# Kernel optimization log

Measured on AMD Instinct MI355X. Metric: run time of the kernel, lower is better.

## Reference

```python
import jax, jax.numpy as jnp
import numpy as np

N_NODES = 50000


def gcn_conv(x, W, b, src, dst, n_nodes):
    """PyG GCNConv: add self-loops, symmetric deg normalization, x@W then aggregate."""
    h = x @ W  # [N, out]
    # add self loops
    loop = jnp.arange(n_nodes, dtype=src.dtype)
    s = jnp.concatenate([src, loop])
    d = jnp.concatenate([dst, loop])
    # degree at target nodes (includes self loop)
    deg = jax.ops.segment_sum(jnp.ones_like(d, dtype=h.dtype), d, num_segments=n_nodes)
    dinv = jnp.where(deg > 0, jax.lax.rsqrt(deg), 0.0)
    norm = dinv[s] * dinv[d]  # [E+N]
    msgs = h[s] * norm[:, None]  # [E+N, out]
    out = jax.ops.segment_sum(msgs, d, num_segments=n_nodes)
    return out + b


def setup_inputs() -> dict:
    key = jax.random.key(0)
    k = jax.random.split(key, 8)
    d_in, d_h, d_z = 128, 128, 32
    x = jax.random.normal(k[0], (N_NODES, d_in), dtype=jnp.float32)
    edge_index = jax.random.randint(k[1], (2, 600000), 0, N_NODES, dtype=jnp.int64)
    y_edge_index = jax.random.randint(k[2], (2, 200000), 0, N_NODES, dtype=jnp.int64)
    W1 = jax.random.normal(k[3], (d_in, d_h), dtype=jnp.float32) / np.sqrt(d_in)
    b1 = jnp.zeros((d_h,), dtype=jnp.float32)
    W_mu = jax.random.normal(k[4], (d_h, d_z), dtype=jnp.float32) / np.sqrt(d_h)
    b_mu = jnp.zeros((d_z,), dtype=jnp.float32)
    W_ls = jax.random.normal(k[5], (d_h, d_z), dtype=jnp.float32) / np.sqrt(d_h)
    b_ls = jnp.zeros((d_z,), dtype=jnp.float32)
    return {"x": x, "edge_index": edge_index, "y_edge_index": y_edge_index,
            "W1": W1, "b1": b1, "W_mu": W_mu, "b_mu": b_mu, "W_ls": W_ls, "b_ls": b_ls}


def reference(x, edge_index, y_edge_index, W1, b1, W_mu, b_mu, W_ls, b_ls):
    ei = jnp.concatenate([edge_index, y_edge_index], axis=1)
    src, dst = ei[0], ei[1]
    n = x.shape[0]
    h = jax.nn.relu(gcn_conv(x, W1, b1, src, dst, n))
    z_mu = gcn_conv(h, W_mu, b_mu, src, dst, n)
    z_logstd = gcn_conv(h, W_ls, b_ls, src, dst, n)
    return (z_mu, z_logstd)
```

## Files before the change

### kernel.cpp

```cpp
#include <hip/hip_runtime.h>
#include <hip/hip_bf16.h>

#define CAP 64
#define NODES_PER_BLOCK 4

typedef __attribute__((ext_vector_type(8))) short short8;
typedef __attribute__((ext_vector_type(4))) float f32x4;

__device__ __forceinline__ unsigned short f2bf(float f) {
    unsigned int u = __float_as_uint(f);
    unsigned int r = (u + 0x7fffu + ((u >> 16) & 1u)) >> 16;
    return (unsigned short)r;
}
__device__ __forceinline__ float bf_lo(unsigned int u) { return __uint_as_float(u << 16); }
__device__ __forceinline__ float bf_hi(unsigned int u) { return __uint_as_float(u & 0xffff0000u); }

__global__ void fill_edges_kernel(const int* __restrict__ e1,
                                  const int* __restrict__ e2,
                                  int* __restrict__ counts, int* __restrict__ edges,
                                  int E1, int E2) {
    int e = blockIdx.x * blockDim.x + threadIdx.x;
    int s, d;
    if (e < E1) {
        s = e1[e]; d = e1[E1 + e];
    } else if (e < E1 + E2) {
        int t = e - E1;
        s = e2[t]; d = e2[E2 + t];
    } else return;
    int pos = atomicAdd(&counts[d], 1);
    if (pos < CAP) edges[d * CAP + pos] = s;
}

__global__ void dinv_kernel(const int* __restrict__ counts, float* __restrict__ dinv, int n) {
    int i = blockIdx.x * blockDim.x + threadIdx.x;
    if (i < n) dinv[i] = rsqrtf((float)(counts[i] + 1));
}

template <typename AT, int NT>
__global__ __launch_bounds__(256) void gemm_mfma_kernel(
    const AT* __restrict__ A, const float* __restrict__ Wa, const float* __restrict__ Wb,
    const float* __restrict__ dinv, unsigned short* __restrict__ C, int M) {
    constexpr int N   = NT * 16;
    constexpr int LDT = 136;
    __shared__ unsigned short As[64 * LDT];
    __shared__ unsigned short Ws[N * LDT];
    int tid  = threadIdx.x;
    int lane = tid & 63, w = tid >> 6;
    int brow = blockIdx.x * 64;

    if constexpr (sizeof(AT) == 4) {
        for (int it = 0; it < 8; ++it) {
            int idx = it * 256 + tid;
            int row = idx >> 5, c4 = idx & 31;
            int gr = brow + row;
            float4 v = make_float4(0.f, 0.f, 0.f, 0.f);
            if (gr < M) v = ((const float4*)(A + (size_t)gr * 128))[c4];
            ushort4 o; o.x = f2bf(v.x); o.y = f2bf(v.y); o.z = f2bf(v.z); o.w = f2bf(v.w);
            *(ushort4*)(As + row * LDT + c4 * 4) = o;
        }
    } else {
        for (int it = 0; it < 4; ++it) {
            int idx = it * 256 + tid;
            int row = idx >> 4, c8 = idx & 15;
            int gr = brow + row;
            short8 v = {};
            if (gr < M) v = ((const short8*)(A + (size_t)gr * 128))[c8];
            *(short8*)(As + row * LDT + c8 * 8) = v;
        }
    }
    if constexpr (NT == 8) {
        for (int it = 0; it < 16; ++it) {
            int idx = it * 256 + tid;
            int k = idx >> 5, q = idx & 31;
            float4 v = ((const float4*)(Wa + (size_t)k * 128))[q];
            int c = q * 4;
            Ws[(c + 0) * LDT + k] = f2bf(v.x);
            Ws[(c + 1) * LDT + k] = f2bf(v.y);
            Ws[(c + 2) * LDT + k] = f2bf(v.z);
            Ws[(c + 3) * LDT + k] = f2bf(v.w);
        }
    } else {
        for (int it = 0; it < 8; ++it) {
            int idx = it * 256 + tid;
            int k = idx >> 4, q = idx & 15;
            float4 v = (q < 8) ? ((const float4*)(Wa + (size_t)k * 32))[q]
                               : ((const float4*)(Wb + (size_t)k * 32))[q - 8];
            int c = q * 4;
            Ws[(c + 0) * LDT + k] = f2bf(v.x);
            Ws[(c + 1) * LDT + k] = f2bf(v.y);
            Ws[(c + 2) * LDT + k] = f2bf(v.z);
            Ws[(c + 3) * LDT + k] = f2bf(v.w);
        }
    }
    __syncthreads();

    f32x4 acc[NT] = {};
    int r = lane & 15, g = lane >> 4;
    const unsigned short* arow = As + (16 * w + r) * LDT + 8 * g;
#pragma unroll
    for (int kk = 0; kk < 4; ++kk) {
        short8 a = *(const short8*)(arow + 32 * kk);
#pragma unroll
        for (int ct = 0; ct < NT; ++ct) {
            short8 b = *(const short8*)(Ws + (ct * 16 + r) * LDT + 32 * kk + 8 * g);
            acc[ct] = __builtin_amdgcn_mfma_f32_16x16x32_bf16(a, b, acc[ct], 0, 0, 0);
        }
    }

#pragma unroll
    for (int ct = 0; ct < NT; ++ct) {
#pragma unroll
        for (int rr = 0; rr < 4; ++rr) {
            int row = brow + 16 * w + 4 * g + rr;
            if (row < M) {
                float sc = dinv[row];
                C[(size_t)row * N + ct * 16 + r] = f2bf(sc * acc[ct][rr]);
            }
        }
    }
}

__global__ void agg_h_kernel(const unsigned short* __restrict__ h1, const int* __restrict__ edges,
                             const int* __restrict__ counts, const float* __restrict__ dinv,
                             const float* __restrict__ b1, unsigned short* __restrict__ h, int n) {
    int wave = threadIdx.x >> 6, lane = threadIdx.x & 63;
    int v = blockIdx.x * NODES_PER_BLOCK + wave;
    if (v >= n) return;
    int cnt = min(counts[v], CAP);
    const int* el = edges + (size_t)v * CAP;
    float ax = 0.f, ay = 0.f;
#pragma unroll 4
    for (int e = 0; e < cnt; ++e) {
        int s = el[e];
        unsigned int u = ((const unsigned int*)(h1 + (size_t)s * 128))[lane];
        ax += bf_lo(u);
        ay += bf_hi(u);
    }
    unsigned int su = ((const unsigned int*)(h1 + (size_t)v * 128))[lane];
    ax += bf_lo(su);
    ay += bf_hi(su);
    float di = dinv[v];
    float ox = di * ax + b1[2 * lane];
    float oy = di * ay + b1[2 * lane + 1];
    unsigned int pack = (unsigned int)f2bf(fmaxf(ox, 0.f)) |
                        ((unsigned int)f2bf(fmaxf(oy, 0.f)) << 16);
    ((unsigned int*)(h + (size_t)v * 128))[lane] = pack;
}

__global__ void agg_out_kernel(const unsigned short* __restrict__ g, const int* __restrict__ edges,
                               const int* __restrict__ counts, const float* __restrict__ dinv,
                               const float* __restrict__ bmu, const float* __restrict__ bls,
                               float* __restrict__ out, int n) {
    int wave = threadIdx.x >> 6, lane = threadIdx.x & 63;
    int v = blockIdx.x * NODES_PER_BLOCK + wave;
    if (v >= n) return;
    int cnt = min(counts[v], CAP);
    const int* el = edges + (size_t)v * CAP;
    float acc = 0.f;
#pragma unroll 4
    for (int e = 0; e < cnt; ++e) {
        int s = el[e];
        acc += __uint_as_float((unsigned int)g[(size_t)s * 64 + lane] << 16);
    }
    acc += __uint_as_float((unsigned int)g[(size_t)v * 64 + lane] << 16);
    float res = dinv[v] * acc;
    if (lane < 32) {
        out[(size_t)v * 32 + lane] = res + bmu[lane];
    } else {
        out[(size_t)n * 32 + (size_t)v * 32 + (lane - 32)] = res + bls[lane - 32];
    }
}

extern "C" void kernel_launch(void* const* d_in, const int* in_sizes, int n_in,
                              void* d_out, int out_size, void* d_ws, size_t ws_size,
                              hipStream_t stream) {
    const float* x   = (const float*)d_in[0];
    const int*   ei  = (const int*)d_in[1];
    const int*   yei = (const int*)d_in[2];
    const float* W1  = (const float*)d_in[3];
    const float* b1  = (const float*)d_in[4];
    const float* Wmu = (const float*)d_in[5];
    const float* bmu = (const float*)d_in[6];
    const float* Wls = (const float*)d_in[7];
    const float* bls = (const float*)d_in[8];

    const int N  = in_sizes[0] / 128;
    const int E1 = in_sizes[1] / 2;
    const int E2 = in_sizes[2] / 2;
    const int E  = E1 + E2;

    size_t off = 0;
    auto alloc = [&](size_t bytes) {
        char* p = (char*)d_ws + off;
        off += (bytes + 255) & ~(size_t)255;
        return (void*)p;
    };
    int*            counts = (int*)alloc((size_t)N * 4);
    float*          dinv   = (float*)alloc((size_t)N * 4);
    int*            edges  = (int*)alloc((size_t)N * CAP * 4);
    unsigned short* h1     = (unsigned short*)alloc((size_t)N * 128 * 2);
    unsigned short* h      = (unsigned short*)alloc((size_t)N * 128 * 2);
    unsigned short* g      = h1;
    (void)ws_size; (void)n_in; (void)out_size;

    const int NB_N = (N + 255) / 256;
    const int NB_E = (E + 255) / 256;
    const int NB_G = (N + 63) / 64;

    hipMemsetAsync(counts, 0, (size_t)N * 4, stream);
    fill_edges_kernel<<<NB_E, 256, 0, stream>>>(ei, yei, counts, edges, E1, E2);
    dinv_kernel<<<NB_N, 256, 0, stream>>>(counts, dinv, N);

    gemm_mfma_kernel<float, 8><<<NB_G, 256, 0, stream>>>(x, W1, nullptr, dinv, h1, N);
    agg_h_kernel<<<(N + NODES_PER_BLOCK - 1) / NODES_PER_BLOCK, 64 * NODES_PER_BLOCK, 0, stream>>>(
        h1, edges, counts, dinv, b1, h, N);

    gemm_mfma_kernel<unsigned short, 4><<<NB_G, 256, 0, stream>>>(h, Wmu, Wls, dinv, g, N);
    agg_out_kernel<<<(N + NODES_PER_BLOCK - 1) / NODES_PER_BLOCK, 64 * NODES_PER_BLOCK, 0, stream>>>(
        g, edges, counts, dinv, bmu, bls, (float*)d_out, N);
}
```

Before: 251.3 us.

## Fuse edge fill with first GEMM, use 16-bit edge lists, inline degree norms

```diff
diff --git a/kernel.cpp b/kernel.cpp
--- a/kernel.cpp
+++ b/kernel.cpp
@@ -15,147 +15,144 @@
 __device__ __forceinline__ float bf_lo(unsigned int u) { return __uint_as_float(u << 16); }
 __device__ __forceinline__ float bf_hi(unsigned int u) { return __uint_as_float(u & 0xffff0000u); }
 
-__global__ void fill_edges_kernel(const int* __restrict__ e1,
-                                  const int* __restrict__ e2,
-                                  int* __restrict__ counts, int* __restrict__ edges,
-                                  int E1, int E2) {
-    int e = blockIdx.x * blockDim.x + threadIdx.x;
-    int s, d;
-    if (e < E1) {
-        s = e1[e]; d = e1[E1 + e];
-    } else if (e < E1 + E2) {
-        int t = e - E1;
-        s = e2[t]; d = e2[E2 + t];
-    } else return;
-    int pos = atomicAdd(&counts[d], 1);
-    if (pos < CAP) edges[d * CAP + pos] = s;
-}
-
-__global__ void dinv_kernel(const int* __restrict__ counts, float* __restrict__ dinv, int n) {
-    int i = blockIdx.x * blockDim.x + threadIdx.x;
-    if (i < n) dinv[i] = rsqrtf((float)(counts[i] + 1));
-}
-
-template <typename AT, int NT>
-__global__ __launch_bounds__(256) void gemm_mfma_kernel(
-    const AT* __restrict__ A, const float* __restrict__ Wa, const float* __restrict__ Wb,
-    const float* __restrict__ dinv, unsigned short* __restrict__ C, int M) {
-    constexpr int N   = NT * 16;
-    constexpr int LDT = 136;
-    __shared__ unsigned short As[64 * LDT];
-    __shared__ unsigned short Ws[N * LDT];
-    int tid  = threadIdx.x;
-    int lane = tid & 63, w = tid >> 6;
-    int brow = blockIdx.x * 64;
-
-    if constexpr (sizeof(AT) == 4) {
-        for (int it = 0; it < 8; ++it) {
-            int idx = it * 256 + tid;
-            int row = idx >> 5, c4 = idx & 31;
-            int gr = brow + row;
-            float4 v = make_float4(0.f, 0.f, 0.f, 0.f);
-            if (gr < M) v = ((const float4*)(A + (size_t)gr * 128))[c4];
-            ushort4 o; o.x = f2bf(v.x); o.y = f2bf(v.y); o.z = f2bf(v.z); o.w = f2bf(v.w);
-            *(ushort4*)(As + row * LDT + c4 * 4) = o;
-        }
+__global__ void prep_wt_kernel(const float* __restrict__ W1, const float* __restrict__ Wmu,
+                               const float* __restrict__ Wls,
+                               unsigned short* __restrict__ W1T, unsigned short* __restrict__ W2T) {
+    int idx = blockIdx.x * 256 + threadIdx.x;
+    if (idx < 128 * 128) {
+        int c = idx >> 7, k = idx & 127;
+        W1T[c * 128 + k] = f2bf(W1[k * 128 + c]);
     } else {
-        for (int it = 0; it < 4; ++it) {
-            int idx = it * 256 + tid;
-            int row = idx >> 4, c8 = idx & 15;
-            int gr = brow + row;
-            short8 v = {};
-            if (gr < M) v = ((const short8*)(A + (size_t)gr * 128))[c8];
-            *(short8*)(As + row * LDT + c8 * 8) = v;
-        }
-    }
-    if constexpr (NT == 8) {
-        for (int it = 0; it < 16; ++it) {
-            int idx = it * 256 + tid;
-            int k = idx >> 5, q = idx & 31;
-            float4 v = ((const float4*)(Wa + (size_t)k * 128))[q];
-            int c = q * 4;
-            Ws[(c + 0) * LDT + k] = f2bf(v.x);
-            Ws[(c + 1) * LDT + k] = f2bf(v.y);
-            Ws[(c + 2) * LDT + k] = f2bf(v.z);
-            Ws[(c + 3) * LDT + k] = f2bf(v.w);
-        }
-    } else {
-        for (int it = 0; it < 8; ++it) {
-            int idx = it * 256 + tid;
-            int k = idx >> 4, q = idx & 15;
-            float4 v = (q < 8) ? ((const float4*)(Wa + (size_t)k * 32))[q]
-                               : ((const float4*)(Wb + (size_t)k * 32))[q - 8];
-            int c = q * 4;
-            Ws[(c + 0) * LDT + k] = f2bf(v.x);
-            Ws[(c + 1) * LDT + k] = f2bf(v.y);
-            Ws[(c + 2) * LDT + k] = f2bf(v.z);
-            Ws[(c + 3) * LDT + k] = f2bf(v.w);
-        }
-    }
-    __syncthreads();
-
-    f32x4 acc[NT] = {};
+        int i2 = idx - 128 * 128;
+        if (i2 < 64 * 128) {
+            int c = i2 >> 7, k = i2 & 127;
+            float v = (c < 32) ? Wmu[k * 32 + c] : Wls[k * 32 + (c - 32)];
+            W2T[c * 128 + k] = f2bf(v);
+        }
+    }
+}
+
+__global__ __launch_bounds__(256) void fused_fill_gemm1(
+    const int* __restrict__ e1, const int* __restrict__ e2,
+    const float* __restrict__ x, const unsigned short* __restrict__ W1T,
+    int* __restrict__ counts, unsigned short* __restrict__ edges,
+    unsigned short* __restrict__ h1, int E1, int E2, int M, int nbe) {
+    int bid = blockIdx.x;
+    if (bid < nbe) {
+        int e = bid * 256 + threadIdx.x;
+        int s, d;
+        if (e < E1) {
+            s = e1[e]; d = e1[E1 + e];
+        } else if (e < E1 + E2) {
+            int t = e - E1;
+            s = e2[t]; d = e2[E2 + t];
+        } else return;
+        int pos = atomicAdd(&counts[d], 1);
+        if (pos < CAP) edges[d * CAP + pos] = (unsigned short)s;
+        return;
+    }
+    int wv = ((bid - nbe) << 2) | (threadIdx.x >> 6);
+    int brow = wv << 4;
+    if (brow >= M) return;
+    int lane = threadIdx.x & 63;
     int r = lane & 15, g = lane >> 4;
-    const unsigned short* arow = As + (16 * w + r) * LDT + 8 * g;
+    const float* ar = x + (size_t)(brow + r) * 128;
+    f32x4 acc[8] = {};
 #pragma unroll
     for (int kk = 0; kk < 4; ++kk) {
-        short8 a = *(const short8*)(arow + 32 * kk);
-#pragma unroll
-        for (int ct = 0; ct < NT; ++ct) {
-            short8 b = *(const short8*)(Ws + (ct * 16 + r) * LDT + 32 * kk + 8 * g);
-            acc[ct] = __builtin_amdgcn_mfma_f32_16x16x32_bf16(a, b, acc[ct], 0, 0, 0);
-        }
-    }
-
-#pragma unroll
-    for (int ct = 0; ct < NT; ++ct) {
+        float4 a0 = *(const float4*)(ar + kk * 32 + g * 8);
+        float4 a1 = *(const float4*)(ar + kk * 32 + g * 8 + 4);
+        short8 af;
+        af[0] = (short)f2bf(a0.x); af[1] = (short)f2bf(a0.y);
+        af[2] = (short)f2bf(a0.z); af[3] = (short)f2bf(a0.w);
+        af[4] = (short)f2bf(a1.x); af[5] = (short)f2bf(a1.y);
+        af[6] = (short)f2bf(a1.z); af[7] = (short)f2bf(a1.w);
+#pragma unroll
+        for (int ct = 0; ct < 8; ++ct) {
+            short8 b = *(const short8*)(W1T + (size_t)(ct * 16 + r) * 128 + kk * 32 + g * 8);
+            acc[ct] = __builtin_amdgcn_mfma_f32_16x16x32_bf16(af, b, acc[ct], 0, 0, 0);
+        }
+    }
+#pragma unroll
+    for (int ct = 0; ct < 8; ++ct) {
 #pragma unroll
         for (int rr = 0; rr < 4; ++rr) {
-            int row = brow + 16 * w + 4 * g + rr;
-            if (row < M) {
-                float sc = dinv[row];
-                C[(size_t)row * N + ct * 16 + r] = f2bf(sc * acc[ct][rr]);
-            }
-        }
-    }
-}
-
-__global__ void agg_h_kernel(const unsigned short* __restrict__ h1, const int* __restrict__ edges,
-                             const int* __restrict__ counts, const float* __restrict__ dinv,
-                             const float* __restrict__ b1, unsigned short* __restrict__ h, int n) {
+            int row = brow + 4 * g + rr;
+            h1[(size_t)row * 128 + ct * 16 + r] = f2bf(acc[ct][rr]);
+        }
+    }
+}
+
+__global__ void agg_h_kernel(const unsigned short* __restrict__ h1,
+                             const unsigned short* __restrict__ edges,
+                             const int* __restrict__ counts, const float* __restrict__ b1,
+                             unsigned short* __restrict__ h, int n) {
     int wave = threadIdx.x >> 6, lane = threadIdx.x & 63;
     int v = blockIdx.x * NODES_PER_BLOCK + wave;
     if (v >= n) return;
-    int cnt = min(counts[v], CAP);
-    const int* el = edges + (size_t)v * CAP;
+    int cv = counts[v];
+    int cnt = min(cv, CAP);
+    const unsigned short* el = edges + (size_t)v * CAP;
     float ax = 0.f, ay = 0.f;
 #pragma unroll 4
     for (int e = 0; e < cnt; ++e) {
         int s = el[e];
+        float w = rsqrtf((float)(counts[s] + 1));
         unsigned int u = ((const unsigned int*)(h1 + (size_t)s * 128))[lane];
-        ax += bf_lo(u);
-        ay += bf_hi(u);
-    }
+        ax = fmaf(w, bf_lo(u), ax);
+        ay = fmaf(w, bf_hi(u), ay);
+    }
+    float di = rsqrtf((float)(cv + 1));
     unsigned int su = ((const unsigned int*)(h1 + (size_t)v * 128))[lane];
-    ax += bf_lo(su);
-    ay += bf_hi(su);
-    float di = dinv[v];
-    float ox = di * ax + b1[2 * lane];
-    float oy = di * ay + b1[2 * lane + 1];
+    float ox = di * fmaf(di, bf_lo(su), ax) + b1[2 * lane];
+    float oy = di * fmaf(di, bf_hi(su), ay) + b1[2 * lane + 1];
     unsigned int pack = (unsigned int)f2bf(fmaxf(ox, 0.f)) |
                         ((unsigned int)f2bf(fmaxf(oy, 0.f)) << 16);
     ((unsigned int*)(h + (size_t)v * 128))[lane] = pack;
 }
 
-__global__ void agg_out_kernel(const unsigned short* __restrict__ g, const int* __restrict__ edges,
-                               const int* __restrict__ counts, const float* __restrict__ dinv,
+__global__ __launch_bounds__(256) void gemm2_kernel(const unsigned short* __restrict__ h,
+                                                    const unsigned short* __restrict__ W2T,
+                                                    const int* __restrict__ counts,
+                                                    unsigned short* __restrict__ g2, int M) {
+    int wv = (blockIdx.x << 2) | (threadIdx.x >> 6);
+    int brow = wv << 4;
+    if (brow >= M) return;
+    int lane = threadIdx.x & 63;
+    int r = lane & 15, g = lane >> 4;
+    const unsigned short* ar = h + (size_t)(brow + r) * 128;
+    f32x4 acc[4] = {};
+#pragma unroll
+    for (int kk = 0; kk < 4; ++kk) {
+        short8 af = *(const short8*)(ar + kk * 32 + g * 8);
+#pragma unroll
+        for (int ct = 0; ct < 4; ++ct) {
+            short8 b = *(const short8*)(W2T + (size_t)(ct * 16 + r) * 128 + kk * 32 + g * 8);
+            acc[ct] = __builtin_amdgcn_mfma_f32_16x16x32_bf16(af, b, acc[ct], 0, 0, 0);
+        }
+    }
+#pragma unroll
+    for (int ct = 0; ct < 4; ++ct) {
+#pragma unroll
+        for (int rr = 0; rr < 4; ++rr) {
+            int row = brow + 4 * g + rr;
+            float sc = rsqrtf((float)(counts[row] + 1));
+            g2[(size_t)row * 64 + ct * 16 + r] = f2bf(sc * acc[ct][rr]);
+        }
+    }
+}
+
+__global__ void agg_out_kernel(const unsigned short* __restrict__ g,
+                               const unsigned short* __restrict__ edges,
+                               const int* __restrict__ counts,
                                const float* __restrict__ bmu, const float* __restrict__ bls,
                                float* __restrict__ out, int n) {
     int wave = threadIdx.x >> 6, lane = threadIdx.x & 63;
     int v = blockIdx.x * NODES_PER_BLOCK + wave;
     if (v >= n) return;
-    int cnt = min(counts[v], CAP);
-    const int* el = edges + (size_t)v * CAP;
+    int cv = counts[v];
+    int cnt = min(cv, CAP);
+    const unsigned short* el = edges + (size_t)v * CAP;
     float acc = 0.f;
 #pragma unroll 4
     for (int e = 0; e < cnt; ++e) {
@@ -163,7 +160,7 @@
         acc += __uint_as_float((unsigned int)g[(size_t)s * 64 + lane] << 16);
     }
     acc += __uint_as_float((unsigned int)g[(size_t)v * 64 + lane] << 16);
-    float res = dinv[v] * acc;
+    float res = rsqrtf((float)(cv + 1)) * acc;
     if (lane < 32) {
         out[(size_t)v * 32 + lane] = res + bmu[lane];
     } else {
@@ -196,26 +193,28 @@
         return (void*)p;
     };
     int*            counts = (int*)alloc((size_t)N * 4);
-    float*          dinv   = (float*)alloc((size_t)N * 4);
-    int*            edges  = (int*)alloc((size_t)N * CAP * 4);
+    unsigned short* edges  = (unsigned short*)alloc((size_t)N * CAP * 2);
     unsigned short* h1     = (unsigned short*)alloc((size_t)N * 128 * 2);
     unsigned short* h      = (unsigned short*)alloc((size_t)N * 128 * 2);
-    unsigned short* g      = h1;
+    unsigned short* g2     = (unsigned short*)alloc((size_t)N * 64 * 2);
+    unsigned short* W1T    = (unsigned short*)alloc(128 * 128 * 2);
+    unsigned short* W2T    = (unsigned short*)alloc(64 * 128 * 2);
     (void)ws_size; (void)n_in; (void)out_size;
 
-    const int NB_N = (N + 255) / 256;
     const int NB_E = (E + 255) / 256;
-    const int NB_G = (N + 63) / 64;
+    const int NB_G1 = (N / 16 + 3) / 4;
+    const int NB_AG = (N + NODES_PER_BLOCK - 1) / NODES_PER_BLOCK;
 
     hipMemsetAsync(counts, 0, (size_t)N * 4, stream);
-    fill_edges_kernel<<<NB_E, 256, 0, stream>>>(ei, yei, counts, edges, E1, E2);
-    dinv_kernel<<<NB_N, 256, 0, stream>>>(counts, dinv, N);
-
-    gemm_mfma_kernel<float, 8><<<NB_G, 256, 0, stream>>>(x, W1, nullptr, dinv, h1, N);
-    agg_h_kernel<<<(N + NODES_PER_BLOCK - 1) / NODES_PER_BLOCK, 64 * NODES_PER_BLOCK, 0, stream>>>(
-        h1, edges, counts, dinv, b1, h, N);
-
-    gemm_mfma_kernel<unsigned short, 4><<<NB_G, 256, 0, stream>>>(h, Wmu, Wls, dinv, g, N);
-    agg_out_kernel<<<(N + NODES_PER_BLOCK - 1) / NODES_PER_BLOCK, 64 * NODES_PER_BLOCK, 0, stream>>>(
-        g, edges, counts, dinv, bmu, bls, (float*)d_out, N);
-}
+    prep_wt_kernel<<<(128 * 128 + 64 * 128 + 255) / 256, 256, 0, stream>>>(W1, Wmu, Wls, W1T, W2T);
+
+    fused_fill_gemm1<<<NB_E + NB_G1, 256, 0, stream>>>(ei, yei, x, W1T, counts, edges, h1,
+                                                       E1, E2, N, NB_E);
+
+    agg_h_kernel<<<NB_AG, 64 * NODES_PER_BLOCK, 0, stream>>>(h1, edges, counts, b1, h, N);
+
+    gemm2_kernel<<<NB_G1, 256, 0, stream>>>(h, W2T, counts, g2, N);
+
+    agg_out_kernel<<<NB_AG, 64 * NODES_PER_BLOCK, 0, stream>>>(g2, edges, counts, bmu, bls,
+                                                               (float*)d_out, N);
+}
```

After: 254.3 us. No clear change (+1.2%).
